# Kernel optimization log

Measured on AMD Instinct MI355X. Metric: run time of the kernel, lower is better.

The kernel has to match this reference:

```python
import jax, jax.numpy as jnp
import numpy as np


def _forward(f2e_emb, score_mat, rel_features, Wk, bk,
             batch_heads, batch_rels, batch_tails, edge_mat, eps):
    B, N, D = f2e_emb.shape
    R = rel_features.shape[0]
    dt = f2e_emb.dtype
    # -cdist(x, x) then row softmax (F.softmax dim=1 on a 2D mat == last axis)
    x2 = jnp.sum(f2e_emb * f2e_emb, axis=-1)                              # [B,N]
    d2 = x2[:, :, None] + x2[:, None, :] - 2.0 * jnp.einsum('bnd,bmd->bnm', f2e_emb, f2e_emb)
    sim = jax.nn.softmax(-jnp.sqrt(jnp.maximum(d2, 0.0)), axis=-1)        # [B,N,N]
    prob = jnp.einsum('bnk,bmk->bnm', sim, score_mat)                     # sim @ score_mat.T
    cand = (prob > eps) & (edge_mat < 1)                                  # candidate (row,col) pairs
    # torch.multinomial(sim[row], 1) per candidate pair -> gumbel-max categorical,
    # one independent draw per (b, row, col) over the row's similarity distribution
    logits = jnp.log(sim)[:, :, None, :]                                  # [B,N,1,N]
    s = jax.random.categorical(jax.random.key(42),
                               jax.lax.stop_gradient(jnp.broadcast_to(logits, (B, N, N, N))),
                               axis=-1)                                    # [B,N,N]
    b3 = jnp.arange(B)[:, None, None]
    r3 = jnp.arange(N)[None, :, None]
    c3 = jnp.arange(N)[None, None, :]
    new_rel = edge_mat[b3, s, c3]                                          # [B,N,N]
    valid = (cand & (new_rel != 0)).astype(dt)
    # per-(node, relation) incidence counts: exactly equivalent to the
    # fact2head_mat/fact2tail_mat sparse.mm aggregation of kb_self_linear(rel_features[rel])
    counts = jnp.zeros((B * N * R,), dt)
    counts = counts.at[((b3 * N + r3) * R + new_rel).ravel()].add(valid.ravel())  # new edge -> head
    counts = counts.at[((b3 * N + c3) * R + new_rel).ravel()].add(valid.ravel())  # new edge -> tail
    b2 = jnp.arange(B)[:, None]
    ones = jnp.ones(batch_heads.shape, dt)
    counts = counts.at[((b2 * N + batch_heads) * R + batch_rels).ravel()].add(ones.ravel())
    counts = counts.at[((b2 * N + batch_tails) * R + batch_rels).ravel()].add(ones.ravel())
    counts = counts.reshape(B, N, R)
    Wr = rel_features @ Wk + bk                                            # kb_self_linear(rel_features) [R,O]
    return jax.nn.relu(jnp.einsum('bnr,ro->bno', counts, Wr))              # [B,N,O]


def setup_inputs():
    key = jax.random.key(0)
    ks = jax.random.split(key, 10)
    B, N, D, O, R, E = 8, 256, 256, 256, 512, 8192
    return {
        'f2e_emb': jax.random.normal(ks[0], (B, N, D), jnp.float32),
        'score_mat': jax.random.normal(ks[1], (B, N, N), jnp.float32),
        'rel_features': jax.random.normal(ks[2], (R, D), jnp.float32),
        'Wk': jax.random.normal(ks[3], (D, O), jnp.float32) / np.sqrt(D).astype(np.float32),
        'bk': jnp.zeros((O,), jnp.float32),
        'local_entity': jax.random.randint(ks[4], (B, N), 0, N, jnp.int32),
        'batch_heads': jax.random.randint(ks[5], (B, E), 0, N, jnp.int32),
        'batch_rels': jax.random.randint(ks[6], (B, E), 0, R, jnp.int32),
        'batch_tails': jax.random.randint(ks[7], (B, E), 0, N, jnp.int32),
        'edge_mat': jax.random.randint(ks[8], (B, N, N), 0, 4, jnp.int32),
        'eps': 0,
    }


def reference(f2e_emb, score_mat, rel_features, Wk, bk, local_entity,
              batch_heads, batch_rels, batch_tails, edge_mat, eps):
    return _forward(f2e_emb, score_mat, rel_features, Wk, bk,
                    batch_heads, batch_rels, batch_tails, edge_mat, eps)
```

## Files before the change

kernel.cpp:

```cpp
#include <hip/hip_runtime.h>
#include <stdint.h>

#define B 8
#define N 256
#define D 256
#define O 256
#define R 512
#define E 8192
#define TR 4
#define TRO 8
#define NSW 8192
#define F32_TINY 1.17549435e-38f

__device__ __forceinline__ void threefry2x32_k42(uint32_t x0, uint32_t x1,
                                                 uint32_t& o0, uint32_t& o1) {
  const uint32_t ks0 = 0u;
  const uint32_t ks1 = 42u;
  const uint32_t ks2 = 0u ^ 42u ^ 0x1BD11BDAu;
  x0 += ks0; x1 += ks1;
#define TF_R(r) { x0 += x1; x1 = (x1 << (r)) | (x1 >> (32 - (r))); x1 ^= x0; }
  TF_R(13) TF_R(15) TF_R(26) TF_R(6)
  x0 += ks1; x1 += ks2 + 1u;
  TF_R(17) TF_R(29) TF_R(16) TF_R(24)
  x0 += ks2; x1 += ks0 + 2u;
  TF_R(13) TF_R(15) TF_R(26) TF_R(6)
  x0 += ks0; x1 += ks1 + 3u;
  TF_R(17) TF_R(29) TF_R(16) TF_R(24)
  x0 += ks1; x1 += ks2 + 4u;
  TF_R(13) TF_R(15) TF_R(26) TF_R(6)
  x0 += ks2; x1 += ks0 + 5u;
#undef TF_R
  o0 = x0; o1 = x1;
}

__device__ __forceinline__ float gumbel_from_bits_f(float f) {
  float u = (f == 0.0f) ? F32_TINY : f;
  return -logf(-logf(u));
}

__global__ __launch_bounds__(256) void prep_kernel(const float* __restrict__ score,
                                                   float* __restrict__ scoreT,
                                                   const float* __restrict__ f2e,
                                                   float* __restrict__ f2eT,
                                                   const float* __restrict__ relf,
                                                   const float* __restrict__ Wk,
                                                   const float* __restrict__ bk,
                                                   float* __restrict__ Wr,
                                                   int* __restrict__ wcount) {
  int blk = blockIdx.x;
  if (blk == 0 && threadIdx.x == 0) *wcount = 0;
  if (blk < 256) {
    __shared__ float tile[64][65];
    const float* src = (blk < 128) ? score : f2e;
    float* dst = (blk < 128) ? scoreT : f2eT;
    int b7 = blk & 127;
    int bb = b7 >> 4, t = b7 & 15, ti = t >> 2, tj = t & 3;
    size_t base = (size_t)bb * 65536;
    int c = threadIdx.x & 63, r4 = threadIdx.x >> 6;
#pragma unroll
    for (int rr = 0; rr < 64; rr += 4) {
      int row = rr + r4;
      tile[row][c] = src[base + (size_t)(ti * 64 + row) * 256 + tj * 64 + c];
    }
    __syncthreads();
#pragma unroll
    for (int rr = 0; rr < 64; rr += 4) {
      int row = rr + r4;
      dst[base + (size_t)(tj * 64 + row) * 256 + ti * 64 + c] = tile[c][row];
    }
  } else {
    __shared__ float rrow[TR][D];
    int r0 = (blk - 256) * TR;
    int o = threadIdx.x;
#pragma unroll
    for (int r = 0; r < TR; ++r) rrow[r][o] = relf[(size_t)(r0 + r) * D + o];
    __syncthreads();
    double acc[TR] = {0, 0, 0, 0};
    for (int d = 0; d < D; d += 4) {
      float w0 = Wk[(size_t)(d + 0) * O + o];
      float w1 = Wk[(size_t)(d + 1) * O + o];
      float w2 = Wk[(size_t)(d + 2) * O + o];
      float w3 = Wk[(size_t)(d + 3) * O + o];
#pragma unroll
      for (int r = 0; r < TR; ++r) {
        float4 a = *(const float4*)&rrow[r][d];
        acc[r] += (double)a.x * w0; acc[r] += (double)a.y * w1;
        acc[r] += (double)a.z * w2; acc[r] += (double)a.w * w3;
      }
    }
    float bv = bk[o];
#pragma unroll
    for (int r = 0; r < TR; ++r) Wr[(size_t)(r0 + r) * O + o] = (float)acc[r] + bv;
  }
}

__global__ __launch_bounds__(256) void simcand_kernel(const float* __restrict__ f2e,
                                                      const float* __restrict__ f2eT,
                                                      const float* __restrict__ scoreT,
                                                      const int* __restrict__ edge,
                                                      const int* __restrict__ epsp,
                                                      float* __restrict__ logits,
                                                      float* __restrict__ laux,
                                                      int* __restrict__ wlist,
                                                      int* __restrict__ wcount) {
  int bn0 = blockIdx.x * TR;
  int b = bn0 >> 8;
  int tid = threadIdx.x, lane = tid & 63, w = tid >> 6;
  __shared__ float arow[TR][256];
  __shared__ float nbuf[TR][256];
  __shared__ float x2s[256];
#pragma unroll
  for (int r = 0; r < TR; ++r) arow[r][tid] = f2e[(size_t)(bn0 + r) * 256 + tid];
  __syncthreads();
  double acc[TR] = {0, 0, 0, 0};
  double ax2 = 0.0;
  const float* fT = f2eT + (size_t)b * 65536 + tid;
  for (int dd = 0; dd < 256; dd += 4) {
    float b0 = fT[(size_t)(dd + 0) * 256];
    float b1 = fT[(size_t)(dd + 1) * 256];
    float b2 = fT[(size_t)(dd + 2) * 256];
    float b3 = fT[(size_t)(dd + 3) * 256];
    ax2 += (double)b0 * b0; ax2 += (double)b1 * b1;
    ax2 += (double)b2 * b2; ax2 += (double)b3 * b3;
#pragma unroll
    for (int r = 0; r < TR; ++r) {
      float4 a = *(const float4*)&arow[r][dd];
      acc[r] += (double)a.x * b0; acc[r] += (double)a.y * b1;
      acc[r] += (double)a.z * b2; acc[r] += (double)a.w * b3;
    }
  }
  float x2c = (float)ax2;
  x2s[tid] = x2c;
  __syncthreads();
#pragma unroll
  for (int r = 0; r < TR; ++r) {
    float x2r = x2s[(bn0 + r) & 255];
    float d2 = (x2r + x2c) - 2.0f * (float)acc[r];
    nbuf[r][tid] = -sqrtf(fmaxf(d2, 0.0f));
  }
  __syncthreads();
  {
    float v0 = nbuf[w][lane], v1 = nbuf[w][lane + 64],
          v2 = nbuf[w][lane + 128], v3 = nbuf[w][lane + 192];
    float mx = fmaxf(fmaxf(v0, v1), fmaxf(v2, v3));
#pragma unroll
    for (int off = 32; off > 0; off >>= 1) mx = fmaxf(mx, __shfl_xor(mx, off));
    float p0 = expf(v0 - mx), p1 = expf(v1 - mx), p2 = expf(v2 - mx), p3 = expf(v3 - mx);
    double sd = (double)p0 + (double)p1 + (double)p2 + (double)p3;
#pragma unroll
    for (int off = 32; off > 0; off >>= 1) sd += __shfl_xor(sd, off);
    float denom = (float)sd;
    float s0 = p0 / denom, s1 = p1 / denom, s2 = p2 / denom, s3 = p3 / denom;
    arow[w][lane] = s0; arow[w][lane + 64] = s1;
    arow[w][lane + 128] = s2; arow[w][lane + 192] = s3;
    float l0 = logf(s0), l1 = logf(s1), l2 = logf(s2), l3 = logf(s3);
    size_t rb = (size_t)(bn0 + w) * 256;
    logits[rb + lane] = l0; logits[rb + lane + 64] = l1;
    logits[rb + lane + 128] = l2; logits[rb + lane + 192] = l3;
    int dm = (bn0 + w) & 255;
    int dj = dm >> 6, dl = dm & 63;
    float e0 = (dj == 0 && lane == dl) ? -3.4e38f : l0;
    float e1 = (dj == 1 && lane == dl) ? -3.4e38f : l1;
    float e2 = (dj == 2 && lane == dl) ? -3.4e38f : l2;
    float e3 = (dj == 3 && lane == dl) ? -3.4e38f : l3;
    float Lm = fmaxf(fmaxf(e0, e1), fmaxf(e2, e3));
#pragma unroll
    for (int off = 32; off > 0; off >>= 1) Lm = fmaxf(Lm, __shfl_xor(Lm, off));
    float lown = (dj == 0) ? l0 : (dj == 1) ? l1 : (dj == 2) ? l2 : l3;
    float l_n = __shfl(lown, dl);
    if (lane == 0) {
      laux[2 * (bn0 + w) + 0] = l_n;
      laux[2 * (bn0 + w) + 1] = Lm;
    }
  }
  __syncthreads();
  double acc2[TR] = {0, 0, 0, 0};
  const float* sT = scoreT + (size_t)b * 65536 + tid;
  for (int kk = 0; kk < 256; kk += 4) {
    float b0 = sT[(size_t)(kk + 0) * 256];
    float b1 = sT[(size_t)(kk + 1) * 256];
    float b2 = sT[(size_t)(kk + 2) * 256];
    float b3 = sT[(size_t)(kk + 3) * 256];
#pragma unroll
    for (int r = 0; r < TR; ++r) {
      float4 a = *(const float4*)&arow[r][kk];
      acc2[r] += (double)a.x * b0; acc2[r] += (double)a.y * b1;
      acc2[r] += (double)a.z * b2; acc2[r] += (double)a.w * b3;
    }
  }
  float epsv = (float)epsp[0];
#pragma unroll
  for (int r = 0; r < TR; ++r) {
    int row = (bn0 + r) * 256 + tid;
    int em = edge[(size_t)row];
    bool active = ((float)acc2[r] > epsv) && (em < 1);
    unsigned long long mask = __ballot(active);
    int cnt = __popcll(mask);
    int basev = 0;
    if (lane == 0 && cnt) basev = atomicAdd(wcount, cnt);
    basev = __shfl(basev, 0);
    if (active) {
      int pos = basev + __popcll(mask & ((1ull << lane) - 1ull));
      wlist[pos] = row;
    }
  }
}

__global__ __launch_bounds__(256) void sample_kernel(const float* __restrict__ logits,
                                                     const float* __restrict__ laux,
                                                     const int* __restrict__ wlist,
                                                     const int* __restrict__ wcount,
                                                     const int* __restrict__ edge,
                                                     const int* __restrict__ heads,
                                                     const int* __restrict__ rels,
                                                     const int* __restrict__ tails,
                                                     float* __restrict__ counts) {
  int blk = blockIdx.x;
  if (blk >= 2048) {
    int i = (blk - 2048) * 256 + threadIdx.x;
    int b = i >> 13;
    int h = heads[i], r = rels[i], t = tails[i];
    atomicAdd(&counts[(size_t)(b * N + h) * R + r], 1.0f);
    atomicAdd(&counts[(size_t)(b * N + t) * R + r], 1.0f);
    return;
  }
  int lane = threadIdx.x & 63;
  int gw = blk * 4 + (threadIdx.x >> 6);
  int cnt = *wcount;
  for (int idx = gw; idx < cnt; idx += NSW) {
    int row = wlist[idx];
    int b = row >> 16;
    int n = (row >> 8) & 255;
    int c = row & 255;
    uint32_t base = (uint32_t)row << 8;
    float u0, u1, u2, u3;
    {
      uint32_t a0, a1;
#define GEN_U(q, dst)                                                     \
      threefry2x32_k42(0u, base + (uint32_t)((q) * 64 + lane), a0, a1);    \
      dst = __uint_as_float((((a0 ^ a1) >> 9)) | 0x3f800000u) - 1.0f;
      GEN_U(0, u0) GEN_U(1, u1) GEN_U(2, u2) GEN_U(3, u3)
#undef GEN_U
    }
    float l_n  = laux[2 * ((b << 8) + n) + 0];
    float Lmax = laux[2 * ((b << 8) + n) + 1];
    int qo = n >> 6;
    float uo = (qo == 0) ? u0 : (qo == 1) ? u1 : (qo == 2) ? u2 : u3;
    float u_n = __shfl(uo, n & 63);
    float v_n = gumbel_from_bits_f(u_n) + l_n;
    float thr_g = (v_n - Lmax) - 0.125f;
    float u_thr = expf(-expf(-thr_g));
    bool owner = (lane == (n & 63));
    bool anyc = ((u0 > u_thr) && !(owner && qo == 0)) |
                ((u1 > u_thr) && !(owner && qo == 1)) |
                ((u2 > u_thr) && !(owner && qo == 2)) |
                ((u3 > u_thr) && !(owner && qo == 3));
    if (!__any(anyc)) continue;

    const float* lrow = logits + (size_t)((b << 8) + n) * N;
    float bestv = -1e30f;
    int besti = 0;
    for (int q = 0; q < 4; ++q) {
      int k = q * 64 + lane;
      uint32_t o0, o1;
      threefry2x32_k42(0u, base + (uint32_t)k, o0, o1);
      uint32_t bits = o0 ^ o1;
      float f = __uint_as_float((bits >> 9) | 0x3f800000u) - 1.0f;
      float g = gumbel_from_bits_f(f);
      float v = g + lrow[k];
      if (v > bestv || (v == bestv && k < besti)) { bestv = v; besti = k; }
    }
    for (int off = 32; off > 0; off >>= 1) {
      float ov = __shfl_down(bestv, off);
      int oi = __shfl_down(besti, off);
      if (ov > bestv || (ov == bestv && oi < besti)) { bestv = ov; besti = oi; }
    }
    if (lane == 0) {
      int nr = edge[(size_t)((b << 8) + besti) * N + c];
      if (nr != 0) {
        atomicAdd(&counts[(size_t)((b << 8) + n) * R + nr], 1.0f);
        atomicAdd(&counts[(size_t)((b << 8) + c) * R + nr], 1.0f);
      }
    }
  }
}

__global__ __launch_bounds__(256) void out_kernel(const float* __restrict__ counts,
                                                  const float* __restrict__ Wr,
                                                  float* __restrict__ out) {
  int bn0 = blockIdx.x * TRO;
  int o = threadIdx.x;
  __shared__ float crow[TRO][R];
#pragma unroll
  for (int r = 0; r < TRO; ++r) {
    crow[r][o] = counts[(size_t)(bn0 + r) * R + o];
    crow[r][o + 256] = counts[(size_t)(bn0 + r) * R + 256 + o];
  }
  __syncthreads();
  float acc[TRO] = {0, 0, 0, 0, 0, 0, 0, 0};
  for (int k = 0; k < R; k += 4) {
    float w0 = Wr[(size_t)(k + 0) * O + o];
    float w1 = Wr[(size_t)(k + 1) * O + o];
    float w2 = Wr[(size_t)(k + 2) * O + o];
    float w3 = Wr[(size_t)(k + 3) * O + o];
#pragma unroll
    for (int r = 0; r < TRO; ++r) {
      float4 cv = *(const float4*)&crow[r][k];
      acc[r] += cv.x * w0; acc[r] += cv.y * w1;
      acc[r] += cv.z * w2; acc[r] += cv.w * w3;
    }
  }
#pragma unroll
  for (int r = 0; r < TRO; ++r)
    out[(size_t)(bn0 + r) * O + o] = fmaxf(acc[r], 0.0f);
}

extern "C" void kernel_launch(void* const* d_in, const int* in_sizes, int n_in,
                              void* d_out, int out_size, void* d_ws, size_t ws_size,
                              hipStream_t stream) {
  (void)in_sizes; (void)n_in; (void)out_size; (void)ws_size;
  const float* f2e   = (const float*)d_in[0];
  const float* score = (const float*)d_in[1];
  const float* relf  = (const float*)d_in[2];
  const float* Wk    = (const float*)d_in[3];
  const float* bk    = (const float*)d_in[4];
  const int* heads   = (const int*)d_in[6];
  const int* rels    = (const int*)d_in[7];
  const int* tails   = (const int*)d_in[8];
  const int* edge    = (const int*)d_in[9];
  const int* epsp    = (const int*)d_in[10];
  float* out = (float*)d_out;

  float* ws     = (float*)d_ws;
  float* logits = ws;
  float* Wr     = logits + 524288;
  float* counts = Wr + 131072;
  float* scoreT = counts;
  float* f2eT   = counts + 524288;
  float* laux   = counts + 1048576;
  int*   wlist  = (int*)(laux + 4096);
  int*   wcount = wlist + 524288;

  prep_kernel<<<384, 256, 0, stream>>>(score, scoreT, f2e, f2eT,
                                       relf, Wk, bk, Wr, wcount);
  simcand_kernel<<<(B * N) / TR, 256, 0, stream>>>(f2e, f2eT, scoreT, edge, epsp,
                                                   logits, laux, wlist, wcount);
  hipMemsetAsync(counts, 0, (size_t)B * N * R * sizeof(float), stream);
  sample_kernel<<<2048 + 256, 256, 0, stream>>>(logits, laux, wlist, wcount, edge,
                                                heads, rels, tails, counts);
  out_kernel<<<(B * N) / TRO, 256, 0, stream>>>(counts, Wr, out);
}
```

Before: 214.1 us.

## Switch GEMV paths from double to float and split sim/cand into separate kernels

Replaces the double-precision accumulations in the Wr, similarity and probability matmuls with float accumulation using dual accumulators and register prefetch of the next eight rows. The simcand kernel is split into sim and cand kernels, with x2 norms precomputed in prep. Blocks grow to 512 threads, and the K dimension is split across two halves in Wr and out_kernel. Dropping FP64 removes slow double-rate arithmetic on the GPU. The cost is an extra launch, an extra global round trip for sim, and float rounding that could flip borderline candidate or argmax decisions.

```diff
diff --git a/kernel.cpp b/kernel.cpp
--- a/kernel.cpp
+++ b/kernel.cpp
@@ -7,8 +7,6 @@
 #define O 256
 #define R 512
 #define E 8192
-#define TR 4
-#define TRO 8
 #define NSW 8192
 #define F32_TINY 1.17549435e-38f
 
@@ -38,7 +36,7 @@
   return -logf(-logf(u));
 }
 
-__global__ __launch_bounds__(256) void prep_kernel(const float* __restrict__ score,
+__global__ __launch_bounds__(512) void prep_kernel(const float* __restrict__ score,
                                                    float* __restrict__ scoreT,
                                                    const float* __restrict__ f2e,
                                                    float* __restrict__ f2eT,
@@ -46,9 +44,11 @@
                                                    const float* __restrict__ Wk,
                                                    const float* __restrict__ bk,
                                                    float* __restrict__ Wr,
+                                                   float* __restrict__ x2,
                                                    int* __restrict__ wcount) {
   int blk = blockIdx.x;
-  if (blk == 0 && threadIdx.x == 0) *wcount = 0;
+  int tid = threadIdx.x;
+  if (blk == 0 && tid == 0) *wcount = 0;
   if (blk < 256) {
     __shared__ float tile[64][65];
     const float* src = (blk < 128) ? score : f2e;
@@ -56,90 +56,117 @@
     int b7 = blk & 127;
     int bb = b7 >> 4, t = b7 & 15, ti = t >> 2, tj = t & 3;
     size_t base = (size_t)bb * 65536;
-    int c = threadIdx.x & 63, r4 = threadIdx.x >> 6;
-#pragma unroll
-    for (int rr = 0; rr < 64; rr += 4) {
-      int row = rr + r4;
+    int c = tid & 63, r8 = tid >> 6;
+#pragma unroll
+    for (int rr = 0; rr < 64; rr += 8) {
+      int row = rr + r8;
       tile[row][c] = src[base + (size_t)(ti * 64 + row) * 256 + tj * 64 + c];
     }
     __syncthreads();
 #pragma unroll
-    for (int rr = 0; rr < 64; rr += 4) {
-      int row = rr + r4;
+    for (int rr = 0; rr < 64; rr += 8) {
+      int row = rr + r8;
       dst[base + (size_t)(tj * 64 + row) * 256 + ti * 64 + c] = tile[c][row];
     }
+  } else if (blk < 768) {
+    int r = blk - 256;
+    int o = tid & 255, kh = tid >> 8;
+    __shared__ float rrow[256];
+    __shared__ float part[2][256];
+    if (tid < 256) rrow[tid] = relf[(size_t)r * 256 + tid];
+    __syncthreads();
+    const float* wp = Wk + (size_t)kh * 128 * 256 + o;
+    const float* rp = rrow + kh * 128;
+    float accA = 0.f, accB = 0.f;
+    float nb[8];
+#pragma unroll
+    for (int j = 0; j < 8; ++j) nb[j] = wp[(size_t)j * 256];
+    for (int d = 0; d < 128; d += 8) {
+      float bb[8];
+#pragma unroll
+      for (int j = 0; j < 8; ++j) bb[j] = nb[j];
+      if (d + 8 < 128) {
+#pragma unroll
+        for (int j = 0; j < 8; ++j) nb[j] = wp[(size_t)(d + 8 + j) * 256];
+      }
+#pragma unroll
+      for (int j = 0; j < 8; j += 2) {
+        accA += rp[d + j] * bb[j];
+        accB += rp[d + j + 1] * bb[j + 1];
+      }
+    }
+    part[kh][o] = accA + accB;
+    __syncthreads();
+    if (kh == 0) Wr[(size_t)r * 256 + o] = part[0][o] + part[1][o] + bk[o];
   } else {
-    __shared__ float rrow[TR][D];
-    int r0 = (blk - 256) * TR;
-    int o = threadIdx.x;
-#pragma unroll
-    for (int r = 0; r < TR; ++r) rrow[r][o] = relf[(size_t)(r0 + r) * D + o];
-    __syncthreads();
-    double acc[TR] = {0, 0, 0, 0};
-    for (int d = 0; d < D; d += 4) {
-      float w0 = Wk[(size_t)(d + 0) * O + o];
-      float w1 = Wk[(size_t)(d + 1) * O + o];
-      float w2 = Wk[(size_t)(d + 2) * O + o];
-      float w3 = Wk[(size_t)(d + 3) * O + o];
-#pragma unroll
-      for (int r = 0; r < TR; ++r) {
-        float4 a = *(const float4*)&rrow[r][d];
-        acc[r] += (double)a.x * w0; acc[r] += (double)a.y * w1;
-        acc[r] += (double)a.z * w2; acc[r] += (double)a.w * w3;
-      }
-    }
-    float bv = bk[o];
-#pragma unroll
-    for (int r = 0; r < TR; ++r) Wr[(size_t)(r0 + r) * O + o] = (float)acc[r] + bv;
-  }
-}
-
-__global__ __launch_bounds__(256) void simcand_kernel(const float* __restrict__ f2e,
-                                                      const float* __restrict__ f2eT,
-                                                      const float* __restrict__ scoreT,
-                                                      const int* __restrict__ edge,
-                                                      const int* __restrict__ epsp,
-                                                      float* __restrict__ logits,
-                                                      float* __restrict__ laux,
-                                                      int* __restrict__ wlist,
-                                                      int* __restrict__ wcount) {
-  int bn0 = blockIdx.x * TR;
+    int i = (blk - 768) * 512 + tid;
+    const float4* p = (const float4*)(f2e + (size_t)i * D);
+    double s = 0.0;
+    for (int d = 0; d < D / 4; ++d) {
+      float4 v = p[d];
+      s += (double)v.x * v.x; s += (double)v.y * v.y;
+      s += (double)v.z * v.z; s += (double)v.w * v.w;
+    }
+    x2[i] = (float)s;
+  }
+}
+
+__global__ __launch_bounds__(512) void sim_kernel(const float* __restrict__ f2e,
+                                                  const float* __restrict__ f2eT,
+                                                  const float* __restrict__ x2,
+                                                  float* __restrict__ sim,
+                                                  float* __restrict__ logits,
+                                                  float* __restrict__ laux) {
+  int bn0 = blockIdx.x * 4;
   int b = bn0 >> 8;
-  int tid = threadIdx.x, lane = tid & 63, w = tid >> 6;
-  __shared__ float arow[TR][256];
-  __shared__ float nbuf[TR][256];
-  __shared__ float x2s[256];
-#pragma unroll
-  for (int r = 0; r < TR; ++r) arow[r][tid] = f2e[(size_t)(bn0 + r) * 256 + tid];
+  int tid = threadIdx.x;
+  int col = tid & 255, half = tid >> 8;
+  __shared__ float arow[4][256];
+  __shared__ float nbuf[4][256];
+  {
+    const float2* src = (const float2*)(f2e + (size_t)bn0 * 256);
+    float2 v = src[tid];
+    int rr = tid >> 7, cc = (tid & 127) * 2;
+    arow[rr][cc] = v.x; arow[rr][cc + 1] = v.y;
+  }
   __syncthreads();
-  double acc[TR] = {0, 0, 0, 0};
-  double ax2 = 0.0;
-  const float* fT = f2eT + (size_t)b * 65536 + tid;
-  for (int dd = 0; dd < 256; dd += 4) {
-    float b0 = fT[(size_t)(dd + 0) * 256];
-    float b1 = fT[(size_t)(dd + 1) * 256];
-    float b2 = fT[(size_t)(dd + 2) * 256];
-    float b3 = fT[(size_t)(dd + 3) * 256];
-    ax2 += (double)b0 * b0; ax2 += (double)b1 * b1;
-    ax2 += (double)b2 * b2; ax2 += (double)b3 * b3;
-#pragma unroll
-    for (int r = 0; r < TR; ++r) {
-      float4 a = *(const float4*)&arow[r][dd];
-      acc[r] += (double)a.x * b0; acc[r] += (double)a.y * b1;
-      acc[r] += (double)a.z * b2; acc[r] += (double)a.w * b3;
-    }
-  }
-  float x2c = (float)ax2;
-  x2s[tid] = x2c;
+  int r0 = half * 2, r1 = r0 + 1;
+  const float* fT = f2eT + (size_t)b * 65536 + col;
+  float a0A = 0.f, a0B = 0.f, a1A = 0.f, a1B = 0.f;
+  float nb[8];
+#pragma unroll
+  for (int j = 0; j < 8; ++j) nb[j] = fT[(size_t)j * 256];
+  for (int dd = 0; dd < 256; dd += 8) {
+    float bb[8];
+#pragma unroll
+    for (int j = 0; j < 8; ++j) bb[j] = nb[j];
+    if (dd + 8 < 256) {
+#pragma unroll
+      for (int j = 0; j < 8; ++j) nb[j] = fT[(size_t)(dd + 8 + j) * 256];
+    }
+    float4 p0 = *(const float4*)&arow[r0][dd];
+    float4 p1 = *(const float4*)&arow[r0][dd + 4];
+    float4 q0 = *(const float4*)&arow[r1][dd];
+    float4 q1 = *(const float4*)&arow[r1][dd + 4];
+    a0A += p0.x * bb[0]; a0B += p0.y * bb[1];
+    a0A += p0.z * bb[2]; a0B += p0.w * bb[3];
+    a0A += p1.x * bb[4]; a0B += p1.y * bb[5];
+    a0A += p1.z * bb[6]; a0B += p1.w * bb[7];
+    a1A += q0.x * bb[0]; a1B += q0.y * bb[1];
+    a1A += q0.z * bb[2]; a1B += q0.w * bb[3];
+    a1A += q1.x * bb[4]; a1B += q1.y * bb[5];
+    a1A += q1.z * bb[6]; a1B += q1.w * bb[7];
+  }
+  float x2c = x2[b * 256 + col];
+  {
+    float d20 = (x2[bn0 + r0] + x2c) - 2.0f * (a0A + a0B);
+    nbuf[r0][col] = -sqrtf(fmaxf(d20, 0.0f));
+    float d21 = (x2[bn0 + r1] + x2c) - 2.0f * (a1A + a1B);
+    nbuf[r1][col] = -sqrtf(fmaxf(d21, 0.0f));
+  }
   __syncthreads();
-#pragma unroll
-  for (int r = 0; r < TR; ++r) {
-    float x2r = x2s[(bn0 + r) & 255];
-    float d2 = (x2r + x2c) - 2.0f * (float)acc[r];
-    nbuf[r][tid] = -sqrtf(fmaxf(d2, 0.0f));
-  }
-  __syncthreads();
-  {
+  if (tid < 256) {
+    int lane = tid & 63, w = tid >> 6;
     float v0 = nbuf[w][lane], v1 = nbuf[w][lane + 64],
           v2 = nbuf[w][lane + 128], v3 = nbuf[w][lane + 192];
     float mx = fmaxf(fmaxf(v0, v1), fmaxf(v2, v3));
@@ -151,10 +178,10 @@
     for (int off = 32; off > 0; off >>= 1) sd += __shfl_xor(sd, off);
     float denom = (float)sd;
     float s0 = p0 / denom, s1 = p1 / denom, s2 = p2 / denom, s3 = p3 / denom;
-    arow[w][lane] = s0; arow[w][lane + 64] = s1;
-    arow[w][lane + 128] = s2; arow[w][lane + 192] = s3;
+    size_t rb = (size_t)(bn0 + w) * 256;
+    sim[rb + lane] = s0; sim[rb + lane + 64] = s1;
+    sim[rb + lane + 128] = s2; sim[rb + lane + 192] = s3;
     float l0 = logf(s0), l1 = logf(s1), l2 = logf(s2), l3 = logf(s3);
-    size_t rb = (size_t)(bn0 + w) * 256;
     logits[rb + lane] = l0; logits[rb + lane + 64] = l1;
     logits[rb + lane + 128] = l2; logits[rb + lane + 192] = l3;
     int dm = (bn0 + w) & 255;
@@ -173,27 +200,61 @@
       laux[2 * (bn0 + w) + 1] = Lm;
     }
   }
+}
+
+__global__ __launch_bounds__(512) void cand_kernel(const float* __restrict__ sim,
+                                                   const float* __restrict__ scoreT,
+                                                   const int* __restrict__ edge,
+                                                   const int* __restrict__ epsp,
+                                                   int* __restrict__ wlist,
+                                                   int* __restrict__ wcount) {
+  int bn0 = blockIdx.x * 4;
+  int b = bn0 >> 8;
+  int tid = threadIdx.x;
+  int col = tid & 255, half = tid >> 8;
+  int lane = tid & 63;
+  __shared__ float srow[4][256];
+  {
+    const float2* src = (const float2*)(sim + (size_t)bn0 * 256);
+    float2 v = src[tid];
+    int rr = tid >> 7, cc = (tid & 127) * 2;
+    srow[rr][cc] = v.x; srow[rr][cc + 1] = v.y;
+  }
   __syncthreads();
-  double acc2[TR] = {0, 0, 0, 0};
-  const float* sT = scoreT + (size_t)b * 65536 + tid;
-  for (int kk = 0; kk < 256; kk += 4) {
-    float b0 = sT[(size_t)(kk + 0) * 256];
-    float b1 = sT[(size_t)(kk + 1) * 256];
-    float b2 = sT[(size_t)(kk + 2) * 256];
-    float b3 = sT[(size_t)(kk + 3) * 256];
-#pragma unroll
-    for (int r = 0; r < TR; ++r) {
-      float4 a = *(const float4*)&arow[r][kk];
-      acc2[r] += (double)a.x * b0; acc2[r] += (double)a.y * b1;
-      acc2[r] += (double)a.z * b2; acc2[r] += (double)a.w * b3;
-    }
+  int r0 = half * 2, r1 = r0 + 1;
+  const float* sT = scoreT + (size_t)b * 65536 + col;
+  float a0A = 0.f, a0B = 0.f, a1A = 0.f, a1B = 0.f;
+  float nb[8];
+#pragma unroll
+  for (int j = 0; j < 8; ++j) nb[j] = sT[(size_t)j * 256];
+  for (int kk = 0; kk < 256; kk += 8) {
+    float bb[8];
+#pragma unroll
+    for (int j = 0; j < 8; ++j) bb[j] = nb[j];
+    if (kk + 8 < 256) {
+#pragma unroll
+      for (int j = 0; j < 8; ++j) nb[j] = sT[(size_t)(kk + 8 + j) * 256];
+    }
+    float4 p0 = *(const float4*)&srow[r0][kk];
+    float4 p1 = *(const float4*)&srow[r0][kk + 4];
+    float4 q0 = *(const float4*)&srow[r1][kk];
+    float4 q1 = *(const float4*)&srow[r1][kk + 4];
+    a0A += p0.x * bb[0]; a0B += p0.y * bb[1];
+    a0A += p0.z * bb[2]; a0B += p0.w * bb[3];
+    a0A += p1.x * bb[4]; a0B += p1.y * bb[5];
+    a0A += p1.z * bb[6]; a0B += p1.w * bb[7];
+    a1A += q0.x * bb[0]; a1B += q0.y * bb[1];
+    a1A += q0.z * bb[2]; a1B += q0.w * bb[3];
+    a1A += q1.x * bb[4]; a1B += q1.y * bb[5];
+    a1A += q1.z * bb[6]; a1B += q1.w * bb[7];
   }
   float epsv = (float)epsp[0];
-#pragma unroll
-  for (int r = 0; r < TR; ++r) {
-    int row = (bn0 + r) * 256 + tid;
+  float pr[2] = {a0A + a0B, a1A + a1B};
+#pragma unroll
+  for (int rr = 0; rr < 2; ++rr) {
+    int row = (bn0 + r0 + rr) * 256 + col;
     int em = edge[(size_t)row];
-    bool active = ((float)acc2[r] > epsv) && (em < 1);
+    bool active = (pr[rr] > epsv) && (em < 1);
     unsigned long long mask = __ballot(active);
     int cnt = __popcll(mask);
     int basev = 0;
@@ -285,34 +346,53 @@
   }
 }
 
-__global__ __launch_bounds__(256) void out_kernel(const float* __restrict__ counts,
+__global__ __launch_bounds__(512) void out_kernel(const float* __restrict__ counts,
                                                   const float* __restrict__ Wr,
                                                   float* __restrict__ out) {
-  int bn0 = blockIdx.x * TRO;
-  int o = threadIdx.x;
-  __shared__ float crow[TRO][R];
-#pragma unroll
-  for (int r = 0; r < TRO; ++r) {
-    crow[r][o] = counts[(size_t)(bn0 + r) * R + o];
-    crow[r][o + 256] = counts[(size_t)(bn0 + r) * R + 256 + o];
+  int bn0 = blockIdx.x * 4;
+  int tid = threadIdx.x;
+  int o = tid & 255, kh = tid >> 8;
+  __shared__ float crow[4][512];
+  __shared__ float part[2][4][256];
+  {
+    const float4* src = (const float4*)(counts + (size_t)bn0 * 512);
+    float4 v = src[tid];
+    int rr = tid >> 7, cc = (tid & 127) * 4;
+    *(float4*)&crow[rr][cc] = v;
   }
   __syncthreads();
-  float acc[TRO] = {0, 0, 0, 0, 0, 0, 0, 0};
-  for (int k = 0; k < R; k += 4) {
-    float w0 = Wr[(size_t)(k + 0) * O + o];
-    float w1 = Wr[(size_t)(k + 1) * O + o];
-    float w2 = Wr[(size_t)(k + 2) * O + o];
-    float w3 = Wr[(size_t)(k + 3) * O + o];
-#pragma unroll
-    for (int r = 0; r < TRO; ++r) {
-      float4 cv = *(const float4*)&crow[r][k];
-      acc[r] += cv.x * w0; acc[r] += cv.y * w1;
-      acc[r] += cv.z * w2; acc[r] += cv.w * w3;
-    }
-  }
-#pragma unroll
-  for (int r = 0; r < TRO; ++r)
-    out[(size_t)(bn0 + r) * O + o] = fmaxf(acc[r], 0.0f);
+  const float* wp = Wr + (size_t)kh * 256 * 256 + o;
+  const int kbase = kh * 256;
+  float accA[4] = {0, 0, 0, 0}, accB[4] = {0, 0, 0, 0};
+  float nb[8];
+#pragma unroll
+  for (int j = 0; j < 8; ++j) nb[j] = wp[(size_t)j * 256];
+  for (int k = 0; k < 256; k += 8) {
+    float bb[8];
+#pragma unroll
+    for (int j = 0; j < 8; ++j) bb[j] = nb[j];
+    if (k + 8 < 256) {
+#pragma unroll
+      for (int j = 0; j < 8; ++j) nb[j] = wp[(size_t)(k + 8 + j) * 256];
+    }
+#pragma unroll
+    for (int r = 0; r < 4; ++r) {
+      float4 c0 = *(const float4*)&crow[r][kbase + k];
+      float4 c1 = *(const float4*)&crow[r][kbase + k + 4];
+      accA[r] += c0.x * bb[0]; accB[r] += c0.y * bb[1];
+      accA[r] += c0.z * bb[2]; accB[r] += c0.w * bb[3];
+      accA[r] += c1.x * bb[4]; accB[r] += c1.y * bb[5];
+      accA[r] += c1.z * bb[6]; accB[r] += c1.w * bb[7];
+    }
+  }
+#pragma unroll
+  for (int r = 0; r < 4; ++r) part[kh][r][o] = accA[r] + accB[r];
+  __syncthreads();
+  if (kh == 0) {
+#pragma unroll
+    for (int r = 0; r < 4; ++r)
+      out[(size_t)(bn0 + r) * 256 + o] = fmaxf(part[0][r][o] + part[1][r][o], 0.0f);
+  }
 }
 
 extern "C" void kernel_launch(void* const* d_in, const int* in_sizes, int n_in,
@@ -333,20 +413,22 @@
 
   float* ws     = (float*)d_ws;
   float* logits = ws;
-  float* Wr     = logits + 524288;
+  float* sim    = logits + 524288;
+  float* Wr     = sim + 524288;
   float* counts = Wr + 131072;
   float* scoreT = counts;
   float* f2eT   = counts + 524288;
   float* laux   = counts + 1048576;
-  int*   wlist  = (int*)(laux + 4096);
+  float* x2     = laux + 4096;
+  int*   wlist  = (int*)(x2 + 2048);
   int*   wcount = wlist + 524288;
 
-  prep_kernel<<<384, 256, 0, stream>>>(score, scoreT, f2e, f2eT,
-                                       relf, Wk, bk, Wr, wcount);
-  simcand_kernel<<<(B * N) / TR, 256, 0, stream>>>(f2e, f2eT, scoreT, edge, epsp,
-                                                   logits, laux, wlist, wcount);
+  prep_kernel<<<772, 512, 0, stream>>>(score, scoreT, f2e, f2eT,
+                                       relf, Wk, bk, Wr, x2, wcount);
+  sim_kernel<<<(B * N) / 4, 512, 0, stream>>>(f2e, f2eT, x2, sim, logits, laux);
+  cand_kernel<<<(B * N) / 4, 512, 0, stream>>>(sim, scoreT, edge, epsp, wlist, wcount);
   hipMemsetAsync(counts, 0, (size_t)B * N * R * sizeof(float), stream);
   sample_kernel<<<2048 + 256, 256, 0, stream>>>(logits, laux, wlist, wcount, edge,
                                                 heads, rels, tails, counts);
-  out_kernel<<<(B * N) / TRO, 256, 0, stream>>>(counts, Wr, out);
-}
+  out_kernel<<<(B * N) / 4, 512, 0, stream>>>(counts, Wr, out);
+}
```

New measurement: 281.3 us. 1.31x slower.
